# Kernel tuning notes

Measured on AMD Instinct MI355X. Metric: run time of the kernel, lower is better.

The kernel has to match this reference:

```python
import jax, jax.numpy as jnp
import numpy as np

THRESHOLD = 0.5
NEG_POS_RATIO = 3
ALPHA = 1.0
N_CLASSES = 81


def xy_to_cxcy(xy):
    return jnp.concatenate([(xy[..., :2] + xy[..., 2:]) / 2.0,
                            xy[..., 2:] - xy[..., :2]], axis=-1)


def cxcy_to_xy(cxcy):
    return jnp.concatenate([cxcy[..., :2] - cxcy[..., 2:] / 2.0,
                            cxcy[..., :2] + cxcy[..., 2:] / 2.0], axis=-1)


def cxcy_to_gcxgcy(cxcy, priors_cxcy):
    # SSD encoding with standard variances (0.1 for center, 0.2 for size)
    g_cxcy = (cxcy[..., :2] - priors_cxcy[..., :2]) / (priors_cxcy[..., 2:] / 10.0)
    g_wh = jnp.log(cxcy[..., 2:] / priors_cxcy[..., 2:]) * 5.0
    return jnp.concatenate([g_cxcy, g_wh], axis=-1)


def iou_pairwise(a_xy, b_xy):
    # a_xy: (N, O, 4), b_xy: (P, 4) -> (N, O, P)
    lt = jnp.maximum(a_xy[..., :, None, :2], b_xy[None, None, :, :2])
    rb = jnp.minimum(a_xy[..., :, None, 2:], b_xy[None, None, :, 2:])
    wh = jnp.clip(rb - lt, 0.0)
    inter = wh[..., 0] * wh[..., 1]
    area_a = (a_xy[..., 2] - a_xy[..., 0]) * (a_xy[..., 3] - a_xy[..., 1])
    area_b = (b_xy[:, 2] - b_xy[:, 0]) * (b_xy[:, 3] - b_xy[:, 1])
    union = area_a[..., :, None] + area_b[None, None, :] - inter
    return inter / union


def setup_inputs() -> dict:
    key = jax.random.key(0)
    k1, k2, k3, k4, k5, k6, k7 = jax.random.split(key, 7)
    N, P, C, O = 32, 8732, N_CLASSES, 16
    predicted_locs = jax.random.normal(k1, (N, P, 4), dtype=jnp.float32)
    predicted_scores = jax.random.normal(k2, (N, P, C), dtype=jnp.float32)
    # ground-truth boxes: build valid cxcy then convert to xy in [0, 1]
    b_cxy = jax.random.uniform(k3, (N, O, 2), minval=0.2, maxval=0.8)
    b_wh = jax.random.uniform(k4, (N, O, 2), minval=0.05, maxval=0.3)
    boxes = cxcy_to_xy(jnp.concatenate([b_cxy, b_wh], axis=-1)).astype(jnp.float32)
    labels = jax.random.randint(k5, (N, O), 1, C).astype(jnp.int32)  # 0 = background
    # priors in cxcy, valid (positive wh)
    p_cxy = jax.random.uniform(k6, (P, 2), minval=0.05, maxval=0.95)
    p_wh = jax.random.uniform(k7, (P, 2), minval=0.05, maxval=0.4)
    priors_cxcy = jnp.concatenate([p_cxy, p_wh], axis=-1).astype(jnp.float32)
    return {"predicted_locs": predicted_locs, "predicted_scores": predicted_scores,
            "boxes": boxes, "labels": labels, "priors_cxcy": priors_cxcy}


def reference(predicted_locs, predicted_scores, boxes, labels, priors_cxcy):
    N, P, C = predicted_scores.shape
    O = boxes.shape[1]
    priors_xy = cxcy_to_xy(priors_cxcy)  # (P, 4)

    overlap = iou_pairwise(boxes, priors_xy)            # (N, O, P)
    overlap_for_each_prior = overlap.max(axis=1)        # (N, P)
    object_for_each_prior = overlap.argmax(axis=1)      # (N, P)
    prior_for_each_object = overlap.argmax(axis=2)      # (N, O)

    obj_ids = jnp.arange(O)

    def assign(ofp, ovl, pfo):
        # force each object to be matched to its best prior with overlap 1
        ofp = ofp.at[pfo].set(obj_ids)
        ovl = ovl.at[pfo].set(1.0)
        return ofp, ovl

    object_for_each_prior, overlap_for_each_prior = jax.vmap(assign)(
        object_for_each_prior, overlap_for_each_prior, prior_for_each_object)

    label_for_each_prior = jnp.take_along_axis(labels, object_for_each_prior, axis=1)  # (N, P)
    true_classes = jnp.where(overlap_for_each_prior < THRESHOLD, 0, label_for_each_prior)

    matched_boxes = jnp.take_along_axis(
        boxes, object_for_each_prior[..., None], axis=1)  # (N, P, 4)
    true_locs = cxcy_to_gcxgcy(xy_to_cxcy(matched_boxes), priors_cxcy)

    positive = true_classes != 0                          # (N, P)
    pos_f = positive.astype(predicted_locs.dtype)

    # localization loss (L1, reduction='none' in original despite the name)
    loc_per_prior = jnp.abs(predicted_locs - true_locs).sum(axis=-1)  # (N, P)
    n_pos_total = pos_f.sum()
    loc_loss = (loc_per_prior * pos_f).sum() / (4.0 * n_pos_total)

    # confidence loss (cross entropy per prior)
    logp = jax.nn.log_softmax(predicted_scores, axis=-1)
    ce = -jnp.take_along_axis(logp, true_classes[..., None], axis=-1)[..., 0]  # (N, P)

    conf_loss_pos = (ce * pos_f).sum()
    ce_neg = jnp.where(positive, 0.0, ce)
    ce_neg_sorted = -jnp.sort(-ce_neg, axis=1)            # descending
    n_positives = positive.sum(axis=1)                    # (N,)
    hard = (jnp.arange(P)[None, :] < (NEG_POS_RATIO * n_positives)[:, None]).astype(ce.dtype)
    conf_loss_hard_neg = (ce_neg_sorted * hard).sum()
    conf_loss = (conf_loss_hard_neg + conf_loss_pos) / n_pos_total

    return conf_loss + ALPHA * loc_loss
```

## Files before the change

kernel.cpp:

```cpp
#include <hip/hip_runtime.h>
#include <hip/hip_bf16.h>
#include <stdint.h>

#define BLOCK 256
#define MAXO 64
#define TK_THREADS 1024
#define CK_MAX 4096
#define RBPI 64

__global__ void match_object_kernel(const float* __restrict__ boxes,
                                    const float* __restrict__ priors,
                                    int* __restrict__ pfop,
                                    float* __restrict__ acc, int* __restrict__ n_pos,
                                    unsigned* __restrict__ done, int N, int P, int O) {
    __shared__ unsigned long long swm[4];
    int idx = blockIdx.x, tid = threadIdx.x;
    if (idx == 0) {
        for (int j = tid; j < N; j += BLOCK) n_pos[j] = 0;
        if (tid >= 64 && tid < 67) acc[tid - 64] = 0.f;
        if (tid == 96) *done = 0u;
    }
    const float* b = boxes + (size_t)idx * 4;
    float bx0 = b[0], by0 = b[1], bx1 = b[2], by1 = b[3];
    float areaa = (bx1 - bx0) * (by1 - by0);

    unsigned long long best = 0ULL;
    for (int p = tid; p < P; p += BLOCK) {
        float4 pr = ((const float4*)priors)[p];
        float px0 = pr.x - pr.z * 0.5f, py0 = pr.y - pr.w * 0.5f;
        float px1 = pr.x + pr.z * 0.5f, py1 = pr.y + pr.w * 0.5f;
        float areab = (px1 - px0) * (py1 - py0);
        float ltx = fmaxf(bx0, px0), lty = fmaxf(by0, py0);
        float rbx = fminf(bx1, px1), rby = fminf(by1, py1);
        float wx = fmaxf(rbx - ltx, 0.f), wy = fmaxf(rby - lty, 0.f);
        float inter = wx * wy;
        float iou = inter / (areaa + areab - inter);
        unsigned long long cand = (((unsigned long long)__float_as_uint(iou)) << 32) |
                                  (unsigned long long)(0xFFFFFFFFu - (unsigned)p);
        if (cand > best) best = cand;
    }
    #pragma unroll
    for (int off = 32; off >= 1; off >>= 1) {
        unsigned long long other = __shfl_down(best, off);
        if (other > best) best = other;
    }
    if ((tid & 63) == 0) swm[tid >> 6] = best;
    __syncthreads();
    if (tid == 0) {
        unsigned long long r = swm[0];
        for (int w = 1; w < BLOCK / 64; ++w) if (swm[w] > r) r = swm[w];
        pfop[idx] = (int)(0xFFFFFFFFu - (unsigned)(r & 0xFFFFFFFFull));
    }
}

__global__ void __launch_bounds__(BLOCK)
fused_rowwave_kernel(const float* __restrict__ boxes,
                     const float* __restrict__ priors,
                     const float* __restrict__ locs,
                     const int* __restrict__ labels,
                     const int* __restrict__ pfop,
                     const float* __restrict__ scores,
                     float* __restrict__ ce_neg,
                     float* __restrict__ pb_loc, float* __restrict__ pb_pce,
                     int* __restrict__ pb_npos,
                     int N, int P, int O) {
    int n = blockIdx.y, bx = blockIdx.x, tid = threadIdx.x;
    int w = tid >> 6, lane = tid & 63;
    int wid = bx * 4 + w;
    const int WPI = RBPI * 4;

    float4 box = make_float4(0.f, 0.f, 0.f, 0.f);
    int lab = 0, pf = -1;
    if (lane < O) {
        box = ((const float4*)boxes)[n * O + lane];
        lab = labels[n * O + lane];
        pf  = pfop[n * O + lane];
    }

    float wloc = 0.f, wpce = 0.f; int wnp = 0;
    for (int p = wid; p < P; p += WPI) {
        size_t t = (size_t)n * P + p;
        const float* base = scores + t * 81;
        float x1 = base[lane];
        bool has2 = lane < 17;
        float x2 = has2 ? base[64 + lane] : 0.f;
        float4 pr = ((const float4*)priors)[p];

        float e = __expf(x1) + (has2 ? __expf(x2) : 0.f);
        #pragma unroll
        for (int off = 32; off >= 1; off >>= 1) e += __shfl_xor(e, off);

        float px0 = pr.x - pr.z * 0.5f, py0 = pr.y - pr.w * 0.5f;
        float px1v = pr.x + pr.z * 0.5f, py1v = pr.y + pr.w * 0.5f;
        float areab = (px1v - px0) * (py1v - py0);
        unsigned long long key = 0ULL;
        if (lane < O) {
            float ltx = fmaxf(box.x, px0), lty = fmaxf(box.y, py0);
            float rbx = fminf(box.z, px1v), rby = fminf(box.w, py1v);
            float wx = fmaxf(rbx - ltx, 0.f), wy = fmaxf(rby - lty, 0.f);
            float inter = wx * wy;
            float areao = (box.z - box.x) * (box.w - box.y);
            float iou = inter / (areao + areab - inter);
            key = (((unsigned long long)__float_as_uint(iou)) << 32) |
                  (unsigned long long)(0xFFFFFFFFu - (unsigned)lane);
        }
        #pragma unroll
        for (int off = 32; off >= 1; off >>= 1) {
            unsigned long long o2 = __shfl_xor(key, off);
            if (o2 > key) key = o2;
        }
        int obj = (int)(0xFFFFFFFFu - (unsigned)(key & 0xFFFFFFFFull));
        float ov = __uint_as_float((unsigned)(key >> 32));
        unsigned long long fm = __ballot(pf == p);
        if (fm) { obj = 63 - __builtin_clzll(fm); ov = 1.0f; }
        int tc = (ov < 0.5f) ? 0 : __shfl(lab, obj);

        float l = logf(e);
        float stc = (tc < 64) ? __shfl(x1, tc) : __shfl(x2, tc - 64);
        float ce = l - stc;
        bool pos = (tc != 0);
        if (pos) {
            float bx0 = __shfl(box.x, obj), by0 = __shfl(box.y, obj);
            float bx1 = __shfl(box.z, obj), by1 = __shfl(box.w, obj);
            float4 pl = ((const float4*)locs)[t];
            float cx = (bx0 + bx1) * 0.5f, cy = (by0 + by1) * 0.5f;
            float bw = bx1 - bx0, bh = by1 - by0;
            float g0 = (cx - pr.x) / (pr.z / 10.0f);
            float g1 = (cy - pr.y) / (pr.w / 10.0f);
            float g2 = logf(bw / pr.z) * 5.0f;
            float g3 = logf(bh / pr.w) * 5.0f;
            if (lane == 0) {
                wloc += fabsf(pl.x-g0) + fabsf(pl.y-g1) + fabsf(pl.z-g2) + fabsf(pl.w-g3);
                wpce += ce;
                wnp  += 1;
            }
        }
        if (lane == 0) ce_neg[t] = pos ? 0.f : ce;
    }

    __shared__ float sl[4], sp[4]; __shared__ int sn[4];
    if (lane == 0) { sl[w] = wloc; sp[w] = wpce; sn[w] = wnp; }
    __syncthreads();
    if (tid == 0) {
        pb_loc[n * RBPI + bx]  = (sl[0] + sl[1]) + (sl[2] + sl[3]);
        pb_pce[n * RBPI + bx]  = (sp[0] + sp[1]) + (sp[2] + sp[3]);
        pb_npos[n * RBPI + bx] = sn[0] + sn[1] + sn[2] + sn[3];
    }
}

__global__ void match_prior_kernel(const float* __restrict__ boxes,
                                   const float* __restrict__ priors,
                                   const float* __restrict__ locs,
                                   const int* __restrict__ labels,
                                   const int* __restrict__ pfop,
                                   int* __restrict__ tcarr,
                                   float* __restrict__ acc, int* __restrict__ n_pos,
                                   int N, int P, int O) {
    __shared__ float sbx[MAXO * 4];
    __shared__ float sarea[MAXO];
    __shared__ int   spf[MAXO];
    __shared__ int   slab[MAXO];
    int n = blockIdx.y, tid = threadIdx.x;
    if (tid < O * 4) sbx[tid] = boxes[(size_t)n * O * 4 + tid];
    if (tid >= 128 && tid < 128 + O) spf[tid - 128]  = pfop[n * O + (tid - 128)];
    if (tid >= 192 && tid < 192 + O) slab[tid - 192] = labels[n * O + (tid - 192)];
    __syncthreads();
    if (tid < O)
        sarea[tid] = (sbx[tid*4+2] - sbx[tid*4+0]) * (sbx[tid*4+3] - sbx[tid*4+1]);
    __syncthreads();

    int p = blockIdx.x * BLOCK + tid;
    bool valid = p < P;
    float my_loc = 0.f; int my_pos = 0;
    if (valid) {
        float4 pr = ((const float4*)priors)[p];
        float px0 = pr.x - pr.z * 0.5f, py0 = pr.y - pr.w * 0.5f;
        float px1 = pr.x + pr.z * 0.5f, py1 = pr.y + pr.w * 0.5f;
        float areab = (px1 - px0) * (py1 - py0);

        float best = -1.f; int bo = 0;
        for (int o = 0; o < O; ++o) {
            float ltx = fmaxf(sbx[o*4+0], px0);
            float lty = fmaxf(sbx[o*4+1], py0);
            float rbx = fminf(sbx[o*4+2], px1);
            float rby = fminf(sbx[o*4+3], py1);
            float wx = fmaxf(rbx - ltx, 0.f), wy = fmaxf(rby - lty, 0.f);
            float inter = wx * wy;
            float iou = inter / (sarea[o] + areab - inter);
            if (iou > best) { best = iou; bo = o; }
        }
        int fo = -1;
        for (int o = 0; o < O; ++o) if (spf[o] == p) fo = o;
        int obj; float ov;
        if (fo >= 0) { obj = fo; ov = 1.0f; }
        else         { obj = bo; ov = best; }
        int lab = slab[obj];
        int tc = (ov < 0.5f) ? 0 : lab;
        tcarr[(size_t)n * P + p] = tc;
        if (tc != 0) {
            my_pos = 1;
            float x0 = sbx[obj*4+0], y0 = sbx[obj*4+1], x1 = sbx[obj*4+2], y1 = sbx[obj*4+3];
            float cx = (x0 + x1) * 0.5f, cy = (y0 + y1) * 0.5f;
            float w = x1 - x0, h = y1 - y0;
            float g0 = (cx - pr.x) / (pr.z / 10.0f);
            float g1 = (cy - pr.y) / (pr.w / 10.0f);
            float g2 = logf(w / pr.z) * 5.0f;
            float g3 = logf(h / pr.w) * 5.0f;
            const float* pl = locs + ((size_t)n * P + p) * 4;
            my_loc = fabsf(pl[0]-g0) + fabsf(pl[1]-g1) + fabsf(pl[2]-g2) + fabsf(pl[3]-g3);
        }
    }
    #pragma unroll
    for (int off = 32; off >= 1; off >>= 1) {
        my_loc += __shfl_down(my_loc, off);
        my_pos += __shfl_down(my_pos, off);
    }
    if ((tid & 63) == 0 && my_pos) {
        atomicAdd(&acc[0], my_loc);
        atomicAdd(&n_pos[n], my_pos);
    }
}

__global__ void loss_generic_kernel(const float* __restrict__ scores,
                                    const int* __restrict__ tcarr,
                                    float* __restrict__ ce_neg, float* __restrict__ acc,
                                    int NP, int C) {
    int t = blockIdx.x * blockDim.x + threadIdx.x;
    if (t >= NP) return;
    int tc = tcarr[t];
    const float* s = scores + (size_t)t * C;
    float m = -3.0e38f;
    for (int j = 0; j < C; ++j) m = fmaxf(m, s[j]);
    float l = 0.f, stc = 0.f;
    for (int j = 0; j < C; ++j) {
        float v = s[j];
        l += __expf(v - m);
        if (j == tc) stc = v;
    }
    float ce = m + logf(l) - stc;
    bool pos = (tc != 0);
    ce_neg[t] = pos ? 0.f : ce;
    if (pos) atomicAdd(&acc[1], ce);
}

__global__ void topk_final_kernel(const float* __restrict__ ce_neg,
                                  int* __restrict__ n_pos,
                                  const float* __restrict__ pb_loc,
                                  const float* __restrict__ pb_pce,
                                  const int* __restrict__ pb_npos, int npb,
                                  float* __restrict__ acc, unsigned* __restrict__ done,
                                  int N, int P, unsigned* __restrict__ out) {
    __shared__ unsigned skeys[8732];
    __shared__ int hist[4096];
    __shared__ int part[1024];
    __shared__ int s_tb, s_ca, s_tb2, s_ca2, s_cnt, s_np;
    __shared__ float shf[16];
    int n = blockIdx.x, tid = threadIdx.x;

    int k;
    if (npb > 0) {
        if (tid < 64) {
            float psl = 0.f, psp = 0.f; int psn = 0;
            for (int i = tid; i < npb; i += 64) {
                psl += pb_loc[n * npb + i];
                psp += pb_pce[n * npb + i];
                psn += pb_npos[n * npb + i];
            }
            #pragma unroll
            for (int off = 32; off >= 1; off >>= 1) {
                psl += __shfl_down(psl, off);
                psp += __shfl_down(psp, off);
                psn += __shfl_down(psn, off);
            }
            if (tid == 0) {
                s_np = psn;
                n_pos[n] = psn;
                if (psl != 0.f) atomicAdd(&acc[0], psl);
                if (psp != 0.f) atomicAdd(&acc[1], psp);
            }
        }
        __syncthreads();
        k = 3 * s_np;
    } else {
        k = 3 * n_pos[n];
    }
    if (k > P) k = P;
    float bsum = 0.f;

    if (k > 0) {
        const float* row = ce_neg + (size_t)n * P;
        for (int i = tid; i < P; i += TK_THREADS) skeys[i] = __float_as_uint(row[i]);
        #pragma unroll
        for (int b = 0; b < 4; ++b) hist[tid * 4 + b] = 0;
        __syncthreads();

        for (int i = tid; i < P; i += TK_THREADS) atomicAdd(&hist[skeys[i] >> 20], 1);
        __syncthreads();
        int h0 = hist[tid*4], h1 = hist[tid*4+1], h2 = hist[tid*4+2], h3 = hist[tid*4+3];
        part[tid] = h0 + h1 + h2 + h3;
        __syncthreads();
        for (int s = 1; s < 1024; s <<= 1) {
            int v = part[tid] + ((tid + s < 1024) ? part[tid + s] : 0);
            __syncthreads();
            part[tid] = v;
            __syncthreads();
        }
        int sfx = (tid + 1 < 1024) ? part[tid + 1] : 0;
        int sf3 = sfx, sf2 = sfx + h3, sf1 = sf2 + h2, sf0 = sf1 + h1;
        if (sf0 < k && k <= sf0 + h0) { s_tb = tid*4;   s_ca = sf0; }
        if (sf1 < k && k <= sf1 + h1) { s_tb = tid*4+1; s_ca = sf1; }
        if (sf2 < k && k <= sf2 + h2) { s_tb = tid*4+2; s_ca = sf2; }
        if (sf3 < k && k <= sf3 + h3) { s_tb = tid*4+3; s_ca = sf3; }
        __syncthreads();
        int tb = s_tb, kk = k - s_ca;

        if (tid < 256) part[tid] = 0;
        __syncthreads();
        float ssum = 0.f;
        for (int i = tid; i < P; i += TK_THREADS) {
            unsigned key = skeys[i];
            int bin = key >> 20;
            if (bin > tb) ssum += __uint_as_float(key);
            else if (bin == tb) atomicAdd(&part[(key >> 12) & 255u], 1);
        }
        __syncthreads();
        if (tid < 256) {
            int cum = 0;
            for (int b = tid + 1; b < 256; ++b) cum += part[b];
            int h = part[tid];
            if (cum < kk && kk <= cum + h) { s_tb2 = tid; s_ca2 = cum; }
        }
        if (tid == 0) s_cnt = 0;
        __syncthreads();
        int tb2 = s_tb2, kk2 = kk - s_ca2;

        unsigned* ckeys = (unsigned*)hist;
        for (int i = tid; i < P; i += TK_THREADS) {
            unsigned key = skeys[i];
            if ((int)(key >> 20) == tb) {
                int b2 = (key >> 12) & 255u;
                if (b2 > tb2) ssum += __uint_as_float(key);
                else if (b2 == tb2) {
                    int slot = atomicAdd(&s_cnt, 1);
                    if (slot < CK_MAX) ckeys[slot] = key;
                }
            }
        }
        __syncthreads();
        int m = s_cnt; if (m > CK_MAX) m = CK_MAX;
        for (int i = tid; i < m; i += TK_THREADS) {
            unsigned key = ckeys[i];
            int rank = 0;
            for (int j = 0; j < m; ++j) {
                unsigned kj = ckeys[j];
                rank += (kj > key) || (kj == key && j < i);
            }
            if (rank < kk2) ssum += __uint_as_float(key);
        }
        #pragma unroll
        for (int off = 32; off >= 1; off >>= 1) ssum += __shfl_down(ssum, off);
        __syncthreads();
        if ((tid & 63) == 0) shf[tid >> 6] = ssum;
        __syncthreads();
        float tot = 0.f;
        for (int i = 0; i < 16; ++i) tot += shf[i];
        bsum = tot;
    }

    if (tid == 0) {
        if (bsum != 0.f) atomicAdd(&acc[2], bsum);
        __threadfence();
        unsigned old = atomicAdd(done, 1u);
        if (old == (unsigned)(N - 1)) {
            float a0 = atomicAdd(&acc[0], 0.f);
            float a1 = atomicAdd(&acc[1], 0.f);
            float a2 = atomicAdd(&acc[2], 0.f);
            int tot = 0;
            for (int i = 0; i < N; ++i) tot += n_pos[i];
            float npos = (float)tot;
            float conf = (a2 + a1) / npos;
            float loc  = a0 / (4.f * npos);
            float loss = conf + loc;
            unsigned ub = __float_as_uint(loss);
            unsigned r = (ub + 0x7FFFu + ((ub >> 16) & 1u)) >> 16;
            out[0] = (r << 16) | r;
        }
    }
}

extern "C" void kernel_launch(void* const* d_in, const int* in_sizes, int n_in,
                              void* d_out, int out_size, void* d_ws, size_t ws_size,
                              hipStream_t stream) {
    const float* locs   = (const float*)d_in[0];
    const float* scores = (const float*)d_in[1];
    const float* boxes  = (const float*)d_in[2];
    const int*   labels = (const int*)d_in[3];
    const float* priors = (const float*)d_in[4];

    int P = in_sizes[4] / 4;
    long long NPl = in_sizes[0] / 4;
    int N = (int)(NPl / P);
    int C = (int)((long long)in_sizes[1] / NPl);
    int O = in_sizes[3] / N;
    size_t NP = (size_t)N * P;

    char* ws = (char*)d_ws;
    float*    acc    = (float*)ws;     ws += 16;
    unsigned* done   = (unsigned*)ws;  ws += 16;
    int*      n_pos  = (int*)ws;       ws += (size_t)N * 4;
    int*      pfop   = (int*)ws;       ws += (size_t)N * O * 4;
    float*    pb_loc = (float*)ws;     ws += (size_t)N * RBPI * 4;
    float*    pb_pce = (float*)ws;     ws += (size_t)N * RBPI * 4;
    int*      pb_npos= (int*)ws;       ws += (size_t)N * RBPI * 4;
    int*      tcarr  = (int*)ws;       ws += NP * 4;
    float*    ce_neg = (float*)ws;     ws += NP * 4;

    match_object_kernel<<<N * O, BLOCK, 0, stream>>>(boxes, priors, pfop, acc, n_pos,
                                                     done, N, P, O);
    int npb = 0;
    if (C == 81 && O <= 64) {
        npb = RBPI;
        fused_rowwave_kernel<<<dim3(RBPI, N), BLOCK, 0, stream>>>(
            boxes, priors, locs, labels, pfop, scores, ce_neg,
            pb_loc, pb_pce, pb_npos, N, P, O);
    } else {
        int gx = (P + BLOCK - 1) / BLOCK;
        match_prior_kernel<<<dim3(gx, N), BLOCK, 0, stream>>>(boxes, priors, locs, labels,
                                                              pfop, tcarr, acc, n_pos, N, P, O);
        loss_generic_kernel<<<(int)((NP + BLOCK - 1) / BLOCK), BLOCK, 0, stream>>>(
            scores, tcarr, ce_neg, acc, (int)NP, C);
    }
    topk_final_kernel<<<N, TK_THREADS, 0, stream>>>(ce_neg, n_pos,
                                                    pb_loc, pb_pce, pb_npos, npb,
                                                    acc, done, N, P, (unsigned*)d_out);
}
```

Before: 226.9 us.

## Stage score rows in shared memory and process one prior per thread

Replaces the wave-per-prior fused kernel with a block of 128 threads that cooperatively loads a contiguous chunk of 128 score rows into LDS using coalesced float4 loads. Each thread then handles one prior, computing the softmax sum, IoU matching against boxes held in shared memory, and the per-prior losses serially. This removes the per-prior cross-lane shuffle reductions and the idle lanes (only 17 of 64 lanes active for the second load), and raises the grid from 64 blocks per image to one per 128 priors. In exchange each thread reads 81 values at a stride of 81 floats in LDS (odd stride, so bank conflicts should stay low) and runs an O-length serial IoU loop. The roughly 41KB of shared memory per block caps occupancy.

```diff
diff --git a/kernel.cpp b/kernel.cpp
--- a/kernel.cpp
+++ b/kernel.cpp
@@ -3,10 +3,10 @@
 #include <stdint.h>
 
 #define BLOCK 256
+#define SBLOCK 128
 #define MAXO 64
 #define TK_THREADS 1024
 #define CK_MAX 4096
-#define RBPI 64
 
 __global__ void match_object_kernel(const float* __restrict__ boxes,
                                     const float* __restrict__ priors,
@@ -53,98 +53,115 @@
     }
 }
 
-__global__ void __launch_bounds__(BLOCK)
-fused_rowwave_kernel(const float* __restrict__ boxes,
-                     const float* __restrict__ priors,
-                     const float* __restrict__ locs,
-                     const int* __restrict__ labels,
-                     const int* __restrict__ pfop,
-                     const float* __restrict__ scores,
-                     float* __restrict__ ce_neg,
-                     float* __restrict__ pb_loc, float* __restrict__ pb_pce,
-                     int* __restrict__ pb_npos,
-                     int N, int P, int O) {
+__global__ void __launch_bounds__(SBLOCK)
+fused_staged_kernel(const float* __restrict__ boxes,
+                    const float* __restrict__ priors,
+                    const float* __restrict__ locs,
+                    const int* __restrict__ labels,
+                    const int* __restrict__ pfop,
+                    const float* __restrict__ scores,
+                    float* __restrict__ ce_neg,
+                    float* __restrict__ pb_loc, float* __restrict__ pb_pce,
+                    int* __restrict__ pb_npos,
+                    int N, int P, int O) {
+    __shared__ float4 sstage4[SBLOCK * 81 / 4];
+    __shared__ float sbx[MAXO * 4];
+    __shared__ int   spf[MAXO];
+    __shared__ int   slab[MAXO];
+    __shared__ float sl[2], sp[2]; __shared__ int sn[2];
+    const float* sstage = (const float*)sstage4;
+
     int n = blockIdx.y, bx = blockIdx.x, tid = threadIdx.x;
     int w = tid >> 6, lane = tid & 63;
-    int wid = bx * 4 + w;
-    const int WPI = RBPI * 4;
-
-    float4 box = make_float4(0.f, 0.f, 0.f, 0.f);
-    int lab = 0, pf = -1;
-    if (lane < O) {
-        box = ((const float4*)boxes)[n * O + lane];
-        lab = labels[n * O + lane];
-        pf  = pfop[n * O + lane];
-    }
-
-    float wloc = 0.f, wpce = 0.f; int wnp = 0;
-    for (int p = wid; p < P; p += WPI) {
-        size_t t = (size_t)n * P + p;
-        const float* base = scores + t * 81;
-        float x1 = base[lane];
-        bool has2 = lane < 17;
-        float x2 = has2 ? base[64 + lane] : 0.f;
-        float4 pr = ((const float4*)priors)[p];
-
-        float e = __expf(x1) + (has2 ? __expf(x2) : 0.f);
+    int p0 = bx * SBLOCK;
+    int rows = P - p0; if (rows > SBLOCK) rows = SBLOCK;
+    int p = p0 + tid;
+    bool valid = tid < rows;
+    size_t t = (size_t)n * P + p;
+
+    for (int i = tid; i < O * 4; i += SBLOCK) sbx[i] = boxes[(size_t)n * O * 4 + i];
+    for (int i = tid; i < O; i += SBLOCK) { spf[i] = pfop[n * O + i]; slab[i] = labels[n * O + i]; }
+    float4 pr = make_float4(0.f, 0.f, 1.f, 1.f);
+    float4 pl = make_float4(0.f, 0.f, 0.f, 0.f);
+    if (valid) {
+        pr = ((const float4*)priors)[p];
+        pl = ((const float4*)locs)[t];
+    }
+
+    const float4* chunk = (const float4*)(scores + ((size_t)n * P + p0) * 81);
+    if (rows == SBLOCK) {
         #pragma unroll
-        for (int off = 32; off >= 1; off >>= 1) e += __shfl_xor(e, off);
+        for (int j = 0; j < 20; ++j)
+            sstage4[j * SBLOCK + tid] = chunk[j * SBLOCK + tid];
+        if (tid < 32)
+            sstage4[20 * SBLOCK + tid] = chunk[20 * SBLOCK + tid];
+    } else {
+        int nf4 = rows * 81 / 4;
+        for (int j = 0; j < 21; ++j) {
+            int idx = j * SBLOCK + tid;
+            if (idx < nf4) sstage4[idx] = chunk[idx];
+        }
+    }
+    __syncthreads();
+
+    float my_loc = 0.f, my_pce = 0.f; int my_pos = 0;
+    if (valid) {
+        const float* row = sstage + tid * 81;
+        float e = 0.f;
+        #pragma unroll
+        for (int j = 0; j < 81; ++j) e += __expf(row[j]);
 
         float px0 = pr.x - pr.z * 0.5f, py0 = pr.y - pr.w * 0.5f;
-        float px1v = pr.x + pr.z * 0.5f, py1v = pr.y + pr.w * 0.5f;
-        float areab = (px1v - px0) * (py1v - py0);
-        unsigned long long key = 0ULL;
-        if (lane < O) {
-            float ltx = fmaxf(box.x, px0), lty = fmaxf(box.y, py0);
-            float rbx = fminf(box.z, px1v), rby = fminf(box.w, py1v);
+        float px1 = pr.x + pr.z * 0.5f, py1 = pr.y + pr.w * 0.5f;
+        float areab = (px1 - px0) * (py1 - py0);
+        float best = -1.f; int bo = 0;
+        for (int o = 0; o < O; ++o) {
+            float x0 = sbx[o*4+0], y0 = sbx[o*4+1], x1 = sbx[o*4+2], y1 = sbx[o*4+3];
+            float ltx = fmaxf(x0, px0), lty = fmaxf(y0, py0);
+            float rbx = fminf(x1, px1), rby = fminf(y1, py1);
             float wx = fmaxf(rbx - ltx, 0.f), wy = fmaxf(rby - lty, 0.f);
             float inter = wx * wy;
-            float areao = (box.z - box.x) * (box.w - box.y);
+            float areao = (x1 - x0) * (y1 - y0);
             float iou = inter / (areao + areab - inter);
-            key = (((unsigned long long)__float_as_uint(iou)) << 32) |
-                  (unsigned long long)(0xFFFFFFFFu - (unsigned)lane);
-        }
-        #pragma unroll
-        for (int off = 32; off >= 1; off >>= 1) {
-            unsigned long long o2 = __shfl_xor(key, off);
-            if (o2 > key) key = o2;
-        }
-        int obj = (int)(0xFFFFFFFFu - (unsigned)(key & 0xFFFFFFFFull));
-        float ov = __uint_as_float((unsigned)(key >> 32));
-        unsigned long long fm = __ballot(pf == p);
-        if (fm) { obj = 63 - __builtin_clzll(fm); ov = 1.0f; }
-        int tc = (ov < 0.5f) ? 0 : __shfl(lab, obj);
-
-        float l = logf(e);
-        float stc = (tc < 64) ? __shfl(x1, tc) : __shfl(x2, tc - 64);
-        float ce = l - stc;
+            if (iou > best) { best = iou; bo = o; }
+        }
+        int fo = -1;
+        for (int o = 0; o < O; ++o) if (spf[o] == p) fo = o;
+        int obj; float ov;
+        if (fo >= 0) { obj = fo; ov = 1.0f; }
+        else         { obj = bo; ov = best; }
+        int tc = (ov < 0.5f) ? 0 : slab[obj];
+
+        float stc = row[tc];
+        float ce = logf(e) - stc;
         bool pos = (tc != 0);
+        ce_neg[t] = pos ? 0.f : ce;
         if (pos) {
-            float bx0 = __shfl(box.x, obj), by0 = __shfl(box.y, obj);
-            float bx1 = __shfl(box.z, obj), by1 = __shfl(box.w, obj);
-            float4 pl = ((const float4*)locs)[t];
-            float cx = (bx0 + bx1) * 0.5f, cy = (by0 + by1) * 0.5f;
-            float bw = bx1 - bx0, bh = by1 - by0;
+            my_pce = ce; my_pos = 1;
+            float x0 = sbx[obj*4+0], y0 = sbx[obj*4+1], x1 = sbx[obj*4+2], y1 = sbx[obj*4+3];
+            float cx = (x0 + x1) * 0.5f, cy = (y0 + y1) * 0.5f;
+            float bw = x1 - x0, bh = y1 - y0;
             float g0 = (cx - pr.x) / (pr.z / 10.0f);
             float g1 = (cy - pr.y) / (pr.w / 10.0f);
             float g2 = logf(bw / pr.z) * 5.0f;
             float g3 = logf(bh / pr.w) * 5.0f;
-            if (lane == 0) {
-                wloc += fabsf(pl.x-g0) + fabsf(pl.y-g1) + fabsf(pl.z-g2) + fabsf(pl.w-g3);
-                wpce += ce;
-                wnp  += 1;
-            }
-        }
-        if (lane == 0) ce_neg[t] = pos ? 0.f : ce;
-    }
-
-    __shared__ float sl[4], sp[4]; __shared__ int sn[4];
-    if (lane == 0) { sl[w] = wloc; sp[w] = wpce; sn[w] = wnp; }
+            my_loc = fabsf(pl.x-g0) + fabsf(pl.y-g1) + fabsf(pl.z-g2) + fabsf(pl.w-g3);
+        }
+    }
+
+    #pragma unroll
+    for (int off = 32; off >= 1; off >>= 1) {
+        my_loc += __shfl_down(my_loc, off);
+        my_pce += __shfl_down(my_pce, off);
+        my_pos += __shfl_down(my_pos, off);
+    }
+    if (lane == 0) { sl[w] = my_loc; sp[w] = my_pce; sn[w] = my_pos; }
     __syncthreads();
     if (tid == 0) {
-        pb_loc[n * RBPI + bx]  = (sl[0] + sl[1]) + (sl[2] + sl[3]);
-        pb_pce[n * RBPI + bx]  = (sp[0] + sp[1]) + (sp[2] + sp[3]);
-        pb_npos[n * RBPI + bx] = sn[0] + sn[1] + sn[2] + sn[3];
+        int npb = gridDim.x;
+        pb_loc[n * npb + bx]  = sl[0] + sl[1];
+        pb_pce[n * npb + bx]  = sp[0] + sp[1];
+        pb_npos[n * npb + bx] = sn[0] + sn[1];
     }
 }
 
@@ -403,30 +420,31 @@
     int C = (int)((long long)in_sizes[1] / NPl);
     int O = in_sizes[3] / N;
     size_t NP = (size_t)N * P;
+    int gx = (P + SBLOCK - 1) / SBLOCK;
 
     char* ws = (char*)d_ws;
     float*    acc    = (float*)ws;     ws += 16;
     unsigned* done   = (unsigned*)ws;  ws += 16;
     int*      n_pos  = (int*)ws;       ws += (size_t)N * 4;
     int*      pfop   = (int*)ws;       ws += (size_t)N * O * 4;
-    float*    pb_loc = (float*)ws;     ws += (size_t)N * RBPI * 4;
-    float*    pb_pce = (float*)ws;     ws += (size_t)N * RBPI * 4;
-    int*      pb_npos= (int*)ws;       ws += (size_t)N * RBPI * 4;
+    float*    pb_loc = (float*)ws;     ws += (size_t)N * gx * 4;
+    float*    pb_pce = (float*)ws;     ws += (size_t)N * gx * 4;
+    int*      pb_npos= (int*)ws;       ws += (size_t)N * gx * 4;
     int*      tcarr  = (int*)ws;       ws += NP * 4;
     float*    ce_neg = (float*)ws;     ws += NP * 4;
 
     match_object_kernel<<<N * O, BLOCK, 0, stream>>>(boxes, priors, pfop, acc, n_pos,
                                                      done, N, P, O);
     int npb = 0;
-    if (C == 81 && O <= 64) {
-        npb = RBPI;
-        fused_rowwave_kernel<<<dim3(RBPI, N), BLOCK, 0, stream>>>(
+    if (C == 81 && (P % 4) == 0 && O <= MAXO) {
+        npb = gx;
+        fused_staged_kernel<<<dim3(gx, N), SBLOCK, 0, stream>>>(
             boxes, priors, locs, labels, pfop, scores, ce_neg,
             pb_loc, pb_pce, pb_npos, N, P, O);
     } else {
-        int gx = (P + BLOCK - 1) / BLOCK;
-        match_prior_kernel<<<dim3(gx, N), BLOCK, 0, stream>>>(boxes, priors, locs, labels,
-                                                              pfop, tcarr, acc, n_pos, N, P, O);
+        int gbx = (P + BLOCK - 1) / BLOCK;
+        match_prior_kernel<<<dim3(gbx, N), BLOCK, 0, stream>>>(boxes, priors, locs, labels,
+                                                               pfop, tcarr, acc, n_pos, N, P, O);
         loss_generic_kernel<<<(int)((NP + BLOCK - 1) / BLOCK), BLOCK, 0, stream>>>(
             scores, tcarr, ce_neg, acc, (int)NP, C);
     }
```

Result: faster. 182.3 us, median of 2 (-19.6%).
